# Optimization experiments

Measured on AMD Instinct MI355X. Metric: run time of the kernel, lower is better.

The kernel has to match this reference:

```python
import jax, jax.numpy as jnp
import numpy as np

IN_CH, EMB_D, N_EMB = 3, 64, 512
K = 5  # conv kernel size


def _conv(x, w, b):
    # x: (B,C,H,W), w: (O,I,K,K) -> valid conv, stride 1
    y = jax.lax.conv_general_dilated(x, w, (1, 1), 'VALID',
                                     dimension_numbers=('NCHW', 'OIHW', 'NCHW'))
    return y + b[None, :, None, None]


def _convT(x, w, b):
    # transpose conv, stride 1, kernel K: output H+K-1. w: (I,O,K,K)
    y = jax.lax.conv_transpose(x, w, (1, 1), 'VALID',
                               dimension_numbers=('NCHW', 'IOHW', 'NCHW'))
    return y + b[None, :, None, None]


def setup_inputs() -> dict:
    key = jax.random.key(0)
    ks = jax.random.split(key, 14)
    s = 0.05
    inp = {
        'x': jax.random.normal(ks[0], (32, IN_CH, 128, 128), jnp.float32),
        # encoder params
        'ew1': jax.random.normal(ks[1], (32, IN_CH, K, K), jnp.float32) * s,
        'eb1': jnp.zeros((32,), jnp.float32),
        'ew2': jax.random.normal(ks[2], (32, 32, K, K), jnp.float32) * s,
        'eb2': jnp.zeros((32,), jnp.float32),
        'ew3': jax.random.normal(ks[3], (EMB_D, 32, K, K), jnp.float32) * s,
        'eb3': jnp.zeros((EMB_D,), jnp.float32),
        # decoder params (transpose convs, IOHW layout)
        'dw1': jax.random.normal(ks[4], (EMB_D, 32, K, K), jnp.float32) * s,
        'db1': jnp.zeros((32,), jnp.float32),
        'dw2': jax.random.normal(ks[5], (32, 32, K, K), jnp.float32) * s,
        'db2': jnp.zeros((32,), jnp.float32),
        'dw3': jax.random.normal(ks[6], (32, IN_CH, K, K), jnp.float32) * s,
        'db3': jnp.zeros((IN_CH,), jnp.float32),
        # codebook, init matches source: normal / 1000
        'emb': jax.random.normal(ks[7], (N_EMB, EMB_D), jnp.float32) * 1e-3,
    }
    return inp


def _quantize(z, emb):
    # z: (B,D,H,W) -> channels-last for per-pixel distance to codebook
    zb = jnp.moveaxis(z, 1, -1)                      # (B,H,W,D)
    # squared L2 distances, expanded form (avoids (N,B,H,W,D) blowup)
    d = (jnp.sum(zb * zb, -1, keepdims=True)
         - 2.0 * jnp.einsum('bhwd,nd->bhwn', zb, emb)
         + jnp.sum(emb * emb, -1))                   # (B,H,W,N)
    idx = jnp.argmin(d, axis=-1)                     # (B,H,W)
    q = zb + jax.lax.stop_gradient(emb[idx] - zb)    # straight-through
    return jnp.moveaxis(q, -1, 1), idx


def _forward(x, ew1, eb1, ew2, eb2, ew3, eb3, dw1, db1, dw2, db2, dw3, db3, emb):
    h = jax.nn.selu(_conv(x, ew1, eb1))
    h = jax.nn.selu(_conv(h, ew2, eb2))
    z = _conv(h, ew3, eb3)                           # (B,EMB_D,116,116)
    q, idx = _quantize(z, emb)
    h = jax.nn.selu(_convT(q, dw1, db1))
    h = jax.nn.selu(_convT(h, dw2, db2))
    recon = _convT(h, dw3, db3)                      # (B,IN_CH,128,128)
    return recon, idx


def reference(x, ew1, eb1, ew2, eb2, ew3, eb3, dw1, db1, dw2, db2, dw3, db3, emb):
    return _forward(x, ew1, eb1, ew2, eb2, ew3, eb3, dw1, db1, dw2, db2, dw3, db3, emb)
```

## Files before the change

kernel.cpp:

```cpp
#include <hip/hip_runtime.h>
#include <cmath>

#define BATCH 32

static const size_t N_H2 = 32u*32*120*120;
static const size_t N_Q  = 32u*64*116*116;
static const size_t RECON_FLOATS = 32u*3*128*128;

static const size_t OFF_W1D  = 0;
static const size_t OFF_W2D  = OFF_W1D + 2400*8;
static const size_t OFF_W3D  = OFF_W2D + 25600*8;
static const size_t OFF_W4F  = OFF_W3D + 51200*8;
static const size_t OFF_W5F  = OFF_W4F + 51200*4;
static const size_t OFF_W6F  = OFF_W5F + 25600*4;
static const size_t OFF_EMBD = (OFF_W6F + 2400*4 + 255) & ~(size_t)255;
static const size_t OFF_EN32 = OFF_EMBD + 32768*8;
static const size_t OFF_H2F  = (OFF_EN32 + 512*4 + 255) & ~(size_t)255;
static const size_t OFF_QF   = OFF_H2F + N_H2*4;

__device__ inline double selu64(double r) {
    double neg = 1.6732632423543772848170429916717 * expm1(r);
    return 1.0507009873554804934193349852946 * (r > 0. ? r : neg);
}
__device__ inline float selu32(float r) {
    float neg = 1.6732632423543772848170429916717f * expm1f(r);
    return 1.0507009873554804934193349852946f * (r > 0.f ? r : neg);
}

template<typename TOUT>
__global__ void wtrans_k(const float* __restrict__ w, TOUT* __restrict__ wt,
                         int IC, int OC, int trans) {
    int i = blockIdx.x * 256 + threadIdx.x;
    int tot = IC * OC * 25;
    if (i >= tot) return;
    int o  = i % OC;
    int t  = i / OC;
    int ic = t % IC;  t /= IC;
    int kx = t % 5;
    int ky = t / 5;
    float v;
    if (trans) v = w[(((ic * OC) + o) * 5 + ky) * 5 + kx];
    else       v = w[(((o * IC) + ic) * 5 + ky) * 5 + kx];
    wt[i] = (TOUT)v;
}

__global__ void prep_embd(const float* __restrict__ emb, double* __restrict__ embd,
                          float* __restrict__ En32) {
    int n = blockIdx.x * 256 + threadIdx.x;
    if (n >= 512) return;
    double s = 0.;
    for (int c = 0; c < 64; ++c) {
        double e = (double)emb[n * 64 + c];
        embd[n * 64 + c] = e;
        s = fma(e, e, s);
    }
    En32[n] = (float)s;
}

__global__ __launch_bounds__(256)
void enc12_k(const float* __restrict__ x, const double* __restrict__ w1,
             const float* __restrict__ b1, const double* __restrict__ w2,
             const float* __restrict__ b2, float* __restrict__ h2out) {
    __shared__ float xs[3][24][24];
    __shared__ float h1s[8][20][20];
    const int tid = threadIdx.x;
    const int tx = tid & 15, ty = tid >> 4;
    const int ox0 = blockIdx.x * 16, oy0 = blockIdx.y * 16;
    const int b = blockIdx.z;

    for (int i = tid; i < 3 * 576; i += 256) {
        int ic = i / 576;
        int r  = i - ic * 576;
        int sy = r / 24, sx = r - sy * 24;
        int gy = oy0 + sy, gx = ox0 + sx;
        float v = 0.f;
        if (gy < 128 && gx < 128)
            v = x[((size_t)(b * 3 + ic) * 128 + gy) * 128 + gx];
        xs[ic][sy][sx] = v;
    }

    double acc2[32];
#pragma unroll
    for (int o = 0; o < 32; ++o) acc2[o] = (double)b2[o];

    for (int cc = 0; cc < 4; ++cc) {
        __syncthreads();
        for (int j = tid; j < 8 * 400; j += 256) {
            int ch = j / 400;
            int r  = j - ch * 400;
            int sy = r / 20, sx = r - sy * 20;
            int oc1 = cc * 8 + ch;
            int gy = oy0 + sy, gx = ox0 + sx;
            float hv = 0.f;
            if (gy < 124 && gx < 124) {
                double a = (double)b1[oc1];
#pragma unroll
                for (int ky = 0; ky < 5; ++ky)
#pragma unroll
                    for (int kx = 0; kx < 5; ++kx)
#pragma unroll
                        for (int ic = 0; ic < 3; ++ic)
                            a = fma((double)xs[ic][sy + ky][sx + kx],
                                    w1[((size_t)(ky * 5 + kx) * 3 + ic) * 32 + oc1], a);
                float c32 = (float)a;
                hv = (float)selu64((double)c32);
            }
            h1s[ch][sy][sx] = hv;
        }
        __syncthreads();
        for (int icl = 0; icl < 8; ++icl) {
            int gic = cc * 8 + icl;
#pragma unroll
            for (int ky = 0; ky < 5; ++ky)
#pragma unroll
                for (int kx = 0; kx < 5; ++kx) {
                    double v = (double)h1s[icl][ty + ky][tx + kx];
                    const double* wp = w2 + ((size_t)(ky * 5 + kx) * 32 + gic) * 32;
#pragma unroll
                    for (int o = 0; o < 32; ++o)
                        acc2[o] = fma(v, wp[o], acc2[o]);
                }
        }
    }

    const int y2 = oy0 + ty, x2 = ox0 + tx;
    if (y2 < 120 && x2 < 120) {
#pragma unroll
        for (int o = 0; o < 32; ++o) {
            float c32 = (float)acc2[o];
            h2out[((size_t)(b * 32 + o) * 120 + y2) * 120 + x2]
                = (float)selu64((double)c32);
        }
    }
}

__global__ __launch_bounds__(256)
void conv3vq_k(const float* __restrict__ h2, const double* __restrict__ wt,
               const float* __restrict__ bias, const double* __restrict__ embd,
               const float* __restrict__ En32, const float* __restrict__ embf,
               float* __restrict__ q, float* __restrict__ idxo) {
    __shared__ float slds[16][20][20];
    const int tid = threadIdx.x;
    const int tx = tid & 15, ty = tid >> 4;
    const int ox0 = blockIdx.x * 16, oy0 = blockIdx.y * 16;
    const int b = blockIdx.z;

    double acc[64];
#pragma unroll
    for (int o = 0; o < 64; ++o) acc[o] = (double)bias[o];

    for (int cc = 0; cc < 2; ++cc) {
        __syncthreads();
        for (int i = tid; i < 16 * 400; i += 256) {
            int ic = i / 400;
            int r  = i - ic * 400;
            int sy = r / 20, sx = r - sy * 20;
            int gy = oy0 + sy, gx = ox0 + sx;
            float v = 0.f;
            if (gy < 120 && gx < 120)
                v = h2[((size_t)(b * 32 + cc * 16 + ic) * 120 + gy) * 120 + gx];
            slds[ic][sy][sx] = v;
        }
        __syncthreads();

        for (int ic = 0; ic < 16; ++ic) {
            int gic = cc * 16 + ic;
#pragma unroll
            for (int ky = 0; ky < 5; ++ky)
#pragma unroll
                for (int kx = 0; kx < 5; ++kx) {
                    double v = (double)slds[ic][ty + ky][tx + kx];
                    const double* wp = wt + ((size_t)(ky * 5 + kx) * 32 + gic) * 64;
#pragma unroll
                    for (int o = 0; o < 64; ++o)
                        acc[o] = fma(v, wp[o], acc[o]);
                }
        }
    }

    const int oy = oy0 + ty, ox = ox0 + tx;
    if (oy >= 116 || ox >= 116) return;

    float z32[64];
#pragma unroll
    for (int c = 0; c < 64; ++c) z32[c] = (float)acc[c];

    double Sd = 0.;
#pragma unroll
    for (int c = 0; c < 64; ++c) {
        double zv = (double)z32[c];
        Sd = fma(zv, zv, Sd);
    }
    const float S32 = (float)Sd;

    float bestd = __builtin_huge_valf();
    int best = 0;
    for (int n = 0; n < 512; n += 4) {
        const double* e0 = embd + (size_t)n * 64;
        const double* e1 = e0 + 64;
        const double* e2 = e0 + 128;
        const double* e3 = e0 + 192;
        double G0 = 0., G1 = 0., G2 = 0., G3 = 0.;
#pragma unroll
        for (int c = 0; c < 64; ++c) {
            double zv = (double)z32[c];
            G0 = fma(zv, e0[c], G0);
            G1 = fma(zv, e1[c], G1);
            G2 = fma(zv, e2[c], G2);
            G3 = fma(zv, e3[c], G3);
        }
        float g0 = (float)G0, g1 = (float)G1, g2 = (float)G2, g3 = (float)G3;
        float d0 = (S32 - 2.0f * g0) + En32[n];
        float d1 = (S32 - 2.0f * g1) + En32[n + 1];
        float d2 = (S32 - 2.0f * g2) + En32[n + 2];
        float d3 = (S32 - 2.0f * g3) + En32[n + 3];
        if (d0 < bestd) { bestd = d0; best = n; }
        if (d1 < bestd) { bestd = d1; best = n + 1; }
        if (d2 < bestd) { bestd = d2; best = n + 2; }
        if (d3 < bestd) { bestd = d3; best = n + 3; }
    }

    const float* e = embf + (size_t)best * 64;
#pragma unroll
    for (int c = 0; c < 64; ++c) {
        float zv = z32[c];
        float diff = e[c] - zv;
        q[((size_t)(b * 64 + c) * 116 + oy) * 116 + ox] = zv + diff;
    }
    idxo[((size_t)b * 116 + oy) * 116 + ox] = (float)best;
}

template<int IC, int ICB, int OC, bool DOSELU>
__global__ __launch_bounds__(256)
void deconv5_k(const float* __restrict__ in, const float* __restrict__ wt,
               const float* __restrict__ bias, float* __restrict__ out,
               int Hin, int Win, int Hout, int Wout) {
    constexpr int NCH = IC / ICB;
    __shared__ float slds[ICB][20][20];
    const int tid = threadIdx.x;
    const int tx = tid & 15, ty = tid >> 4;
    const int ox0 = blockIdx.x * 16, oy0 = blockIdx.y * 16;
    const int b = blockIdx.z;

    float acc[OC];
#pragma unroll
    for (int o = 0; o < OC; ++o) acc[o] = bias[o];

    for (int cc = 0; cc < NCH; ++cc) {
        __syncthreads();
        for (int i = tid; i < ICB * 400; i += 256) {
            int ic = i / 400;
            int r  = i - ic * 400;
            int sy = r / 20, sx = r - sy * 20;
            int gy = oy0 - 4 + sy;
            int gx = ox0 - 4 + sx;
            float v = 0.f;
            if (gy >= 0 && gy < Hin && gx >= 0 && gx < Win)
                v = in[((size_t)(b * IC + cc * ICB + ic) * Hin + gy) * Win + gx];
            slds[ic][sy][sx] = v;
        }
        __syncthreads();

        for (int ic = 0; ic < ICB; ++ic) {
            int gic = cc * ICB + ic;
#pragma unroll
            for (int ky = 0; ky < 5; ++ky)
#pragma unroll
                for (int kx = 0; kx < 5; ++kx) {
                    float v = slds[ic][ty + ky][tx + kx];
                    const float* wp = wt + ((size_t)(ky * 5 + kx) * IC + gic) * OC;
#pragma unroll
                    for (int o = 0; o < OC; ++o)
                        acc[o] = fmaf(v, wp[o], acc[o]);
                }
        }
    }

    const int oy = oy0 + ty, ox = ox0 + tx;
    if (oy < Hout && ox < Wout) {
#pragma unroll
        for (int o = 0; o < OC; ++o) {
            float r = acc[o];
            if (DOSELU) r = selu32(r);
            out[((size_t)(b * OC + o) * Hout + oy) * Wout + ox] = r;
        }
    }
}

extern "C" void kernel_launch(void* const* d_in, const int* in_sizes, int n_in,
                              void* d_out, int out_size, void* d_ws, size_t ws_size,
                              hipStream_t stream) {
    const float* x   = (const float*)d_in[0];
    const float* ew1 = (const float*)d_in[1];
    const float* eb1 = (const float*)d_in[2];
    const float* ew2 = (const float*)d_in[3];
    const float* eb2 = (const float*)d_in[4];
    const float* ew3 = (const float*)d_in[5];
    const float* eb3 = (const float*)d_in[6];
    const float* dw1 = (const float*)d_in[7];
    const float* db1 = (const float*)d_in[8];
    const float* dw2 = (const float*)d_in[9];
    const float* db2 = (const float*)d_in[10];
    const float* dw3 = (const float*)d_in[11];
    const float* db3 = (const float*)d_in[12];
    const float* emb = (const float*)d_in[13];

    char* base = (char*)d_ws;
    double* W1D  = (double*)(base + OFF_W1D);
    double* W2D  = (double*)(base + OFF_W2D);
    double* W3D  = (double*)(base + OFF_W3D);
    float*  W4F  = (float*) (base + OFF_W4F);
    float*  W5F  = (float*) (base + OFF_W5F);
    float*  W6F  = (float*) (base + OFF_W6F);
    double* EMBD = (double*)(base + OFF_EMBD);
    float*  EN32 = (float*) (base + OFF_EN32);
    float*  H2F  = (float*) (base + OFF_H2F);
    float*  QF   = (float*) (base + OFF_QF);
    float*  D1   = (float*) (base + OFF_H2F);
    float*  D2   = (float*) (base + OFF_QF);

    float* recon = (float*)d_out;
    float* idxo  = (float*)d_out + RECON_FLOATS;

    wtrans_k<double><<<dim3((2400  + 255) / 256), 256, 0, stream>>>(ew1, W1D,  3, 32, 0);
    wtrans_k<double><<<dim3((25600 + 255) / 256), 256, 0, stream>>>(ew2, W2D, 32, 32, 0);
    wtrans_k<double><<<dim3((51200 + 255) / 256), 256, 0, stream>>>(ew3, W3D, 32, 64, 0);
    wtrans_k<float ><<<dim3((51200 + 255) / 256), 256, 0, stream>>>(dw1, W4F, 64, 32, 1);
    wtrans_k<float ><<<dim3((25600 + 255) / 256), 256, 0, stream>>>(dw2, W5F, 32, 32, 1);
    wtrans_k<float ><<<dim3((2400  + 255) / 256), 256, 0, stream>>>(dw3, W6F, 32,  3, 1);
    prep_embd<<<dim3(2), 256, 0, stream>>>(emb, EMBD, EN32);

    dim3 grd(8, 8, BATCH);

    enc12_k<<<grd, 256, 0, stream>>>(x, W1D, eb1, W2D, eb2, H2F);
    conv3vq_k<<<grd, 256, 0, stream>>>(H2F, W3D, eb3, EMBD, EN32, emb, QF, idxo);

    deconv5_k<64, 32, 32, true ><<<grd, 256, 0, stream>>>(QF, W4F, db1, D1, 116, 116, 120, 120);
    deconv5_k<32, 32, 32, true ><<<grd, 256, 0, stream>>>(D1, W5F, db2, D2, 120, 120, 124, 124);
    deconv5_k<32, 32, 3,  false><<<grd, 256, 0, stream>>>(D2, W6F, db3, recon, 124, 124, 128, 128);
}
```

Measured before the change: 6.908 ms.

## Split conv3 and VQ; two-pass fp32 screen with fp64 refine for argmin

```diff
diff --git a/kernel.cpp b/kernel.cpp
--- a/kernel.cpp
+++ b/kernel.cpp
@@ -16,7 +16,7 @@
 static const size_t OFF_EMBD = (OFF_W6F + 2400*4 + 255) & ~(size_t)255;
 static const size_t OFF_EN32 = OFF_EMBD + 32768*8;
 static const size_t OFF_H2F  = (OFF_EN32 + 512*4 + 255) & ~(size_t)255;
-static const size_t OFF_QF   = OFF_H2F + N_H2*4;
+static const size_t OFF_ZQ   = OFF_H2F + N_H2*4;
 
 __device__ inline double selu64(double r) {
     double neg = 1.6732632423543772848170429916717 * expm1(r);
@@ -57,18 +57,17 @@
     En32[n] = (float)s;
 }
 
-__global__ __launch_bounds__(256)
+__global__ __launch_bounds__(512)
 void enc12_k(const float* __restrict__ x, const double* __restrict__ w1,
              const float* __restrict__ b1, const double* __restrict__ w2,
              const float* __restrict__ b2, float* __restrict__ h2out) {
     __shared__ float xs[3][24][24];
-    __shared__ float h1s[8][20][20];
+    __shared__ float h1s[32][20][20];
     const int tid = threadIdx.x;
-    const int tx = tid & 15, ty = tid >> 4;
     const int ox0 = blockIdx.x * 16, oy0 = blockIdx.y * 16;
     const int b = blockIdx.z;
 
-    for (int i = tid; i < 3 * 576; i += 256) {
+    for (int i = tid; i < 3 * 576; i += 512) {
         int ic = i / 576;
         int r  = i - ic * 576;
         int sy = r / 24, sx = r - sy * 24;
@@ -78,156 +77,197 @@
             v = x[((size_t)(b * 3 + ic) * 128 + gy) * 128 + gx];
         xs[ic][sy][sx] = v;
     }
-
-    double acc2[32];
-#pragma unroll
-    for (int o = 0; o < 32; ++o) acc2[o] = (double)b2[o];
-
-    for (int cc = 0; cc < 4; ++cc) {
-        __syncthreads();
-        for (int j = tid; j < 8 * 400; j += 256) {
-            int ch = j / 400;
-            int r  = j - ch * 400;
-            int sy = r / 20, sx = r - sy * 20;
-            int oc1 = cc * 8 + ch;
-            int gy = oy0 + sy, gx = ox0 + sx;
-            float hv = 0.f;
-            if (gy < 124 && gx < 124) {
-                double a = (double)b1[oc1];
-#pragma unroll
-                for (int ky = 0; ky < 5; ++ky)
-#pragma unroll
-                    for (int kx = 0; kx < 5; ++kx)
-#pragma unroll
-                        for (int ic = 0; ic < 3; ++ic)
-                            a = fma((double)xs[ic][sy + ky][sx + kx],
-                                    w1[((size_t)(ky * 5 + kx) * 3 + ic) * 32 + oc1], a);
-                float c32 = (float)a;
-                hv = (float)selu64((double)c32);
+    __syncthreads();
+
+    for (int j = tid; j < 32 * 400; j += 512) {
+        int ch = j / 400;
+        int r  = j - ch * 400;
+        int sy = r / 20, sx = r - sy * 20;
+        int gy = oy0 + sy, gx = ox0 + sx;
+        float hv = 0.f;
+        if (gy < 124 && gx < 124) {
+            double a = (double)b1[ch];
+#pragma unroll
+            for (int ky = 0; ky < 5; ++ky)
+#pragma unroll
+                for (int kx = 0; kx < 5; ++kx)
+#pragma unroll
+                    for (int ic = 0; ic < 3; ++ic)
+                        a = fma((double)xs[ic][sy + ky][sx + kx],
+                                w1[((size_t)(ky * 5 + kx) * 3 + ic) * 32 + ch], a);
+            float c32 = (float)a;
+            hv = (float)selu64((double)c32);
+        }
+        h1s[ch][sy][sx] = hv;
+    }
+    __syncthreads();
+
+    const int px = tid & 15, py = (tid >> 4) & 15;
+    const int og = (tid >> 8) * 16;
+
+    double acc[16];
+#pragma unroll
+    for (int o = 0; o < 16; ++o) acc[o] = (double)b2[og + o];
+
+    for (int ic = 0; ic < 32; ++ic) {
+#pragma unroll
+        for (int ky = 0; ky < 5; ++ky)
+#pragma unroll
+            for (int kx = 0; kx < 5; ++kx) {
+                double v = (double)h1s[ic][py + ky][px + kx];
+                const double* wp = w2 + ((size_t)(ky * 5 + kx) * 32 + ic) * 32 + og;
+#pragma unroll
+                for (int o = 0; o < 16; ++o)
+                    acc[o] = fma(v, wp[o], acc[o]);
             }
-            h1s[ch][sy][sx] = hv;
-        }
-        __syncthreads();
-        for (int icl = 0; icl < 8; ++icl) {
-            int gic = cc * 8 + icl;
-#pragma unroll
-            for (int ky = 0; ky < 5; ++ky)
-#pragma unroll
-                for (int kx = 0; kx < 5; ++kx) {
-                    double v = (double)h1s[icl][ty + ky][tx + kx];
-                    const double* wp = w2 + ((size_t)(ky * 5 + kx) * 32 + gic) * 32;
-#pragma unroll
-                    for (int o = 0; o < 32; ++o)
-                        acc2[o] = fma(v, wp[o], acc2[o]);
-                }
-        }
-    }
-
-    const int y2 = oy0 + ty, x2 = ox0 + tx;
+    }
+
+    const int y2 = oy0 + py, x2 = ox0 + px;
     if (y2 < 120 && x2 < 120) {
 #pragma unroll
-        for (int o = 0; o < 32; ++o) {
-            float c32 = (float)acc2[o];
-            h2out[((size_t)(b * 32 + o) * 120 + y2) * 120 + x2]
+        for (int o = 0; o < 16; ++o) {
+            float c32 = (float)acc[o];
+            h2out[((size_t)(b * 32 + og + o) * 120 + y2) * 120 + x2]
                 = (float)selu64((double)c32);
         }
     }
 }
 
 __global__ __launch_bounds__(256)
-void conv3vq_k(const float* __restrict__ h2, const double* __restrict__ wt,
-               const float* __restrict__ bias, const double* __restrict__ embd,
-               const float* __restrict__ En32, const float* __restrict__ embf,
-               float* __restrict__ q, float* __restrict__ idxo) {
-    __shared__ float slds[16][20][20];
+void conv3_k(const float* __restrict__ h2, const double* __restrict__ wt,
+             const float* __restrict__ bias, float* __restrict__ z) {
+    __shared__ float h2s[32][12][12];
     const int tid = threadIdx.x;
-    const int tx = tid & 15, ty = tid >> 4;
-    const int ox0 = blockIdx.x * 16, oy0 = blockIdx.y * 16;
+    const int ox0 = blockIdx.x * 8, oy0 = blockIdx.y * 8;
     const int b = blockIdx.z;
 
-    double acc[64];
-#pragma unroll
-    for (int o = 0; o < 64; ++o) acc[o] = (double)bias[o];
-
-    for (int cc = 0; cc < 2; ++cc) {
-        __syncthreads();
-        for (int i = tid; i < 16 * 400; i += 256) {
-            int ic = i / 400;
-            int r  = i - ic * 400;
-            int sy = r / 20, sx = r - sy * 20;
-            int gy = oy0 + sy, gx = ox0 + sx;
-            float v = 0.f;
-            if (gy < 120 && gx < 120)
-                v = h2[((size_t)(b * 32 + cc * 16 + ic) * 120 + gy) * 120 + gx];
-            slds[ic][sy][sx] = v;
-        }
-        __syncthreads();
-
-        for (int ic = 0; ic < 16; ++ic) {
-            int gic = cc * 16 + ic;
-#pragma unroll
-            for (int ky = 0; ky < 5; ++ky)
-#pragma unroll
-                for (int kx = 0; kx < 5; ++kx) {
-                    double v = (double)slds[ic][ty + ky][tx + kx];
-                    const double* wp = wt + ((size_t)(ky * 5 + kx) * 32 + gic) * 64;
-#pragma unroll
-                    for (int o = 0; o < 64; ++o)
-                        acc[o] = fma(v, wp[o], acc[o]);
-                }
-        }
-    }
-
-    const int oy = oy0 + ty, ox = ox0 + tx;
-    if (oy >= 116 || ox >= 116) return;
-
-    float z32[64];
-#pragma unroll
-    for (int c = 0; c < 64; ++c) z32[c] = (float)acc[c];
+    for (int i = tid; i < 32 * 144; i += 256) {
+        int ic = i / 144;
+        int r  = i - ic * 144;
+        int sy = r / 12, sx = r - sy * 12;
+        int gy = oy0 + sy, gx = ox0 + sx;
+        float v = 0.f;
+        if (gy < 120 && gx < 120)
+            v = h2[((size_t)(b * 32 + ic) * 120 + gy) * 120 + gx];
+        h2s[ic][sy][sx] = v;
+    }
+    __syncthreads();
+
+    const int px = tid & 7, py = (tid >> 3) & 7;
+    const int og = (tid >> 6) * 16;
+
+    double acc[16];
+#pragma unroll
+    for (int o = 0; o < 16; ++o) acc[o] = (double)bias[og + o];
+
+    for (int ic = 0; ic < 32; ++ic) {
+#pragma unroll
+        for (int ky = 0; ky < 5; ++ky)
+#pragma unroll
+            for (int kx = 0; kx < 5; ++kx) {
+                double v = (double)h2s[ic][py + ky][px + kx];
+                const double* wp = wt + ((size_t)(ky * 5 + kx) * 32 + ic) * 64 + og;
+#pragma unroll
+                for (int o = 0; o < 16; ++o)
+                    acc[o] = fma(v, wp[o], acc[o]);
+            }
+    }
+
+    const int oy = oy0 + py, ox = ox0 + px;
+    if (oy < 116 && ox < 116) {
+#pragma unroll
+        for (int o = 0; o < 16; ++o)
+            z[((size_t)(b * 64 + og + o) * 116 + oy) * 116 + ox] = (float)acc[o];
+    }
+}
+
+__global__ __launch_bounds__(256)
+void vq2_k(const float* __restrict__ z, float* __restrict__ q,
+           const float* __restrict__ embf, const double* __restrict__ embd,
+           const float* __restrict__ En32, float* __restrict__ idxo) {
+    const int HW = 116 * 116;
+    int p = blockIdx.x * 256 + threadIdx.x;
+    int b = p / HW;
+    int r = p - b * HW;
+    const float* zp = z + (size_t)(b * 64) * HW + r;
+
+    float zc[64];
+#pragma unroll
+    for (int c = 0; c < 64; ++c) zc[c] = zp[(size_t)c * HW];
 
     double Sd = 0.;
 #pragma unroll
     for (int c = 0; c < 64; ++c) {
-        double zv = (double)z32[c];
+        double zv = (double)zc[c];
         Sd = fma(zv, zv, Sd);
     }
     const float S32 = (float)Sd;
+
+    float mmin = __builtin_huge_valf();
+    for (int n = 0; n < 512; n += 4) {
+        const float* e0 = embf + (size_t)n * 64;
+        const float* e1 = e0 + 64;
+        const float* e2 = e0 + 128;
+        const float* e3 = e0 + 192;
+        float G0 = 0.f, G1 = 0.f, G2 = 0.f, G3 = 0.f;
+#pragma unroll
+        for (int c = 0; c < 64; ++c) {
+            float zv = zc[c];
+            G0 = fmaf(zv, e0[c], G0);
+            G1 = fmaf(zv, e1[c], G1);
+            G2 = fmaf(zv, e2[c], G2);
+            G3 = fmaf(zv, e3[c], G3);
+        }
+        float m0 = fmaf(-2.f, G0, En32[n]);
+        float m1 = fmaf(-2.f, G1, En32[n + 1]);
+        float m2 = fmaf(-2.f, G2, En32[n + 2]);
+        float m3 = fmaf(-2.f, G3, En32[n + 3]);
+        mmin = fminf(mmin, fminf(fminf(m0, m1), fminf(m2, m3)));
+    }
+    const float thr = mmin + 4.0e-7f * (S32 + 4.0f);
 
     float bestd = __builtin_huge_valf();
     int best = 0;
     for (int n = 0; n < 512; n += 4) {
-        const double* e0 = embd + (size_t)n * 64;
-        const double* e1 = e0 + 64;
-        const double* e2 = e0 + 128;
-        const double* e3 = e0 + 192;
-        double G0 = 0., G1 = 0., G2 = 0., G3 = 0.;
+        const float* e0 = embf + (size_t)n * 64;
+        const float* e1 = e0 + 64;
+        const float* e2 = e0 + 128;
+        const float* e3 = e0 + 192;
+        float G0 = 0.f, G1 = 0.f, G2 = 0.f, G3 = 0.f;
 #pragma unroll
         for (int c = 0; c < 64; ++c) {
-            double zv = (double)z32[c];
-            G0 = fma(zv, e0[c], G0);
-            G1 = fma(zv, e1[c], G1);
-            G2 = fma(zv, e2[c], G2);
-            G3 = fma(zv, e3[c], G3);
-        }
-        float g0 = (float)G0, g1 = (float)G1, g2 = (float)G2, g3 = (float)G3;
-        float d0 = (S32 - 2.0f * g0) + En32[n];
-        float d1 = (S32 - 2.0f * g1) + En32[n + 1];
-        float d2 = (S32 - 2.0f * g2) + En32[n + 2];
-        float d3 = (S32 - 2.0f * g3) + En32[n + 3];
-        if (d0 < bestd) { bestd = d0; best = n; }
-        if (d1 < bestd) { bestd = d1; best = n + 1; }
-        if (d2 < bestd) { bestd = d2; best = n + 2; }
-        if (d3 < bestd) { bestd = d3; best = n + 3; }
+            float zv = zc[c];
+            G0 = fmaf(zv, e0[c], G0);
+            G1 = fmaf(zv, e1[c], G1);
+            G2 = fmaf(zv, e2[c], G2);
+            G3 = fmaf(zv, e3[c], G3);
+        }
+        float m[4] = { fmaf(-2.f, G0, En32[n]),     fmaf(-2.f, G1, En32[n + 1]),
+                       fmaf(-2.f, G2, En32[n + 2]), fmaf(-2.f, G3, En32[n + 3]) };
+#pragma unroll
+        for (int j = 0; j < 4; ++j) {
+            if (m[j] <= thr) {
+                const double* ed = embd + (size_t)(n + j) * 64;
+                double Gd = 0.;
+#pragma unroll
+                for (int c = 0; c < 64; ++c)
+                    Gd = fma((double)zc[c], ed[c], Gd);
+                float g = (float)Gd;
+                float d = (S32 - 2.0f * g) + En32[n + j];
+                if (d < bestd) { bestd = d; best = n + j; }
+            }
+        }
     }
 
     const float* e = embf + (size_t)best * 64;
+    float* qp = q + (size_t)(b * 64) * HW + r;
 #pragma unroll
     for (int c = 0; c < 64; ++c) {
-        float zv = z32[c];
+        float zv = zc[c];
         float diff = e[c] - zv;
-        q[((size_t)(b * 64 + c) * 116 + oy) * 116 + ox] = zv + diff;
-    }
-    idxo[((size_t)b * 116 + oy) * 116 + ox] = (float)best;
+        qp[(size_t)c * HW] = zv + diff;
+    }
+    idxo[p] = (float)best;
 }
 
 template<int IC, int ICB, int OC, bool DOSELU>
@@ -315,9 +355,9 @@
     double* EMBD = (double*)(base + OFF_EMBD);
     float*  EN32 = (float*) (base + OFF_EN32);
     float*  H2F  = (float*) (base + OFF_H2F);
-    float*  QF   = (float*) (base + OFF_QF);
+    float*  ZQ   = (float*) (base + OFF_ZQ);
     float*  D1   = (float*) (base + OFF_H2F);
-    float*  D2   = (float*) (base + OFF_QF);
+    float*  D2   = (float*) (base + OFF_ZQ);
 
     float* recon = (float*)d_out;
     float* idxo  = (float*)d_out + RECON_FLOATS;
@@ -330,12 +370,14 @@
     wtrans_k<float ><<<dim3((2400  + 255) / 256), 256, 0, stream>>>(dw3, W6F, 32,  3, 1);
     prep_embd<<<dim3(2), 256, 0, stream>>>(emb, EMBD, EN32);
 
-    dim3 grd(8, 8, BATCH);
-
-    enc12_k<<<grd, 256, 0, stream>>>(x, W1D, eb1, W2D, eb2, H2F);
-    conv3vq_k<<<grd, 256, 0, stream>>>(H2F, W3D, eb3, EMBD, EN32, emb, QF, idxo);
-
-    deconv5_k<64, 32, 32, true ><<<grd, 256, 0, stream>>>(QF, W4F, db1, D1, 116, 116, 120, 120);
-    deconv5_k<32, 32, 32, true ><<<grd, 256, 0, stream>>>(D1, W5F, db2, D2, 120, 120, 124, 124);
-    deconv5_k<32, 32, 3,  false><<<grd, 256, 0, stream>>>(D2, W6F, db3, recon, 124, 124, 128, 128);
-}
+    enc12_k<<<dim3(8, 8, BATCH), 512, 0, stream>>>(x, W1D, eb1, W2D, eb2, H2F);
+    conv3_k<<<dim3(15, 15, BATCH), 256, 0, stream>>>(H2F, W3D, eb3, ZQ);
+    {
+        int P = BATCH * 116 * 116;
+        vq2_k<<<dim3(P / 256), 256, 0, stream>>>(ZQ, ZQ, emb, EMBD, EN32, idxo);
+    }
+
+    deconv5_k<64, 32, 32, true ><<<dim3(8, 8, BATCH), 256, 0, stream>>>(ZQ, W4F, db1, D1, 116, 116, 120, 120);
+    deconv5_k<32, 32, 32, true ><<<dim3(8, 8, BATCH), 256, 0, stream>>>(D1, W5F, db2, D2, 120, 120, 124, 124);
+    deconv5_k<32, 32, 3,  false><<<dim3(8, 8, BATCH), 256, 0, stream>>>(D2, W6F, db3, recon, 124, 124, 128, 128);
+}
```

Result: slower. 14.66 ms (+112.2%).
